# Kernel optimization log

Measured on AMD Instinct MI355X. Metric: run time of the kernel, lower is better.

The kernel has to match this reference:

```python
import jax, jax.numpy as jnp
import numpy as np

N_HEADS = 8
HEAD_D = 64


def setup_inputs() -> dict:
    key = jax.random.key(0)
    ks = jax.random.split(key, 7)
    b, ds, dc = 4, 4096, 256
    ls, lc = 512, 512
    inner = N_HEADS * HEAD_D  # 512
    out_dim = 512
    data = jax.random.normal(ks[0], (b, ds, dc), dtype=jnp.float32)
    latent = jax.random.normal(ks[1], (b, ls, lc), dtype=jnp.float32)
    # torch nn.Linear weights are [out_features, in_features]
    Wq = jax.random.normal(ks[2], (inner, lc), dtype=jnp.float32) * (lc ** -0.5)
    Wk = jax.random.normal(ks[3], (inner, dc), dtype=jnp.float32) * (dc ** -0.5)
    Wv = jax.random.normal(ks[4], (inner, dc), dtype=jnp.float32) * (dc ** -0.5)
    Wo = jax.random.normal(ks[5], (out_dim, inner), dtype=jnp.float32) * (inner ** -0.5)
    bo = jax.random.normal(ks[6], (out_dim,), dtype=jnp.float32) * 0.02
    return {"data": data, "latent": latent, "Wq": Wq, "Wk": Wk, "Wv": Wv, "Wo": Wo, "bo": bo}


def reference(data, latent, Wq, Wk, Wv, Wo, bo):
    b, ds, _ = data.shape
    ls = latent.shape[1]
    scale = HEAD_D ** -0.5
    # projections, split into heads
    Q = (latent @ Wq.T).reshape(b, ls, N_HEADS, HEAD_D)  # [b,ls,h,d]
    K = (data @ Wk.T).reshape(b, ds, N_HEADS, HEAD_D)    # [b,ds,h,d]
    V = (data @ Wv.T).reshape(b, ds, N_HEADS, HEAD_D)
    # logits [b, ds, ls, h]; original broadcasts then sums over head_d -> einsum
    logits = jnp.einsum('blhd,bshd->bslh', Q, K) * scale
    # softmax over key axis (dim 1 = ds), matching attn_logits.softmax(1)
    attn = jax.nn.softmax(logits, axis=1)
    # weighted sum over keys: [b, ls, h, d] -> [b, ls, inner]
    out = jnp.einsum('bshd,bslh->blhd', V, attn).reshape(b, ls, N_HEADS * HEAD_D)
    # output Linear (dropout is identity in eval)
    return out @ Wo.T + bo
```

## Files before the change

kernel.cpp:

```cpp
#include <hip/hip_runtime.h>

typedef __bf16 bf16;
typedef __bf16 bf16x8 __attribute__((ext_vector_type(8)));
typedef float  f32x4  __attribute__((ext_vector_type(4)));


__device__ __forceinline__ bf16x8 cvt8(float4 a, float4 b) {
    bf16x8 r;
    r[0] = (bf16)a.x; r[1] = (bf16)a.y; r[2] = (bf16)a.z; r[3] = (bf16)a.w;
    r[4] = (bf16)b.x; r[5] = (bf16)b.y; r[6] = (bf16)b.z; r[7] = (bf16)b.w;
    return r;
}

__global__ __launch_bounds__(256) void proj_kvq(
    const float* __restrict__ data, const float* __restrict__ latent,
    const float* __restrict__ Wk, const float* __restrict__ Wv, const float* __restrict__ Wq,
    bf16* __restrict__ K_b, bf16* __restrict__ Vt_b, bf16* __restrict__ Q_b)
{
    __shared__ bf16 As[128 * 32];
    __shared__ bf16 Bs[128 * 32];
    const int bx = blockIdx.x;
    const float* A; const float* Bm; bf16* outb;
    int Kdim, mode, m0, n0;
    if (bx < 512)       { A = data;   Bm = Wk; outb = K_b;  Kdim = 256; mode = 0; m0 = (bx & 127) * 128;         n0 = (bx >> 7) * 128; }
    else if (bx < 1024) { int t = bx - 512;  A = data;   Bm = Wv; outb = Vt_b; Kdim = 256; mode = 1; m0 = (t & 127) * 128; n0 = (t >> 7) * 128; }
    else                { int t = bx - 1024; A = latent; Bm = Wq; outb = Q_b;  Kdim = 512; mode = 2; m0 = (t & 15) * 128;  n0 = (t >> 4) * 128; }

    const int tid = threadIdx.x;
    const int wave = tid >> 6, lane = tid & 63;
    const int wm = wave >> 1, wn = wave & 1;
    const int l15 = lane & 15, quad = lane >> 4;
    const int rowA = tid >> 2;
    const int c8 = (tid & 3) * 8;

    const float* Arow0 = A + (size_t)(m0 + rowA) * Kdim + c8;
    const float* Arow1 = A + (size_t)(m0 + 64 + rowA) * Kdim + c8;
    const float* Brow0 = Bm + (size_t)(n0 + rowA) * Kdim + c8;
    const float* Brow1 = Bm + (size_t)(n0 + 64 + rowA) * Kdim + c8;

    f32x4 acc[4][4] = {};
    float4 a00, a01, a10, a11, b00, b01, b10, b11;

#define LOADP(k) do { \
        a00 = *(const float4*)(Arow0 + (k));     a01 = *(const float4*)(Arow0 + (k) + 4); \
        a10 = *(const float4*)(Arow1 + (k));     a11 = *(const float4*)(Arow1 + (k) + 4); \
        b00 = *(const float4*)(Brow0 + (k));     b01 = *(const float4*)(Brow0 + (k) + 4); \
        b10 = *(const float4*)(Brow1 + (k));     b11 = *(const float4*)(Brow1 + (k) + 4); \
    } while (0)

    LOADP(0);

    for (int k0 = 0; k0 < Kdim; k0 += 32) {
        __syncthreads();
        *(bf16x8*)(As + (size_t)tid * 8)        = cvt8(a00, a01);
        *(bf16x8*)(As + 2048 + (size_t)tid * 8) = cvt8(a10, a11);
        *(bf16x8*)(Bs + (size_t)tid * 8)        = cvt8(b00, b01);
        *(bf16x8*)(Bs + 2048 + (size_t)tid * 8) = cvt8(b10, b11);
        if (k0 + 32 < Kdim) LOADP(k0 + 32);
        __syncthreads();

        bf16x8 af[4], bfr[4];
        #pragma unroll
        for (int mt = 0; mt < 4; mt++)
            af[mt] = *(const bf16x8*)(As + (wm * 64 + mt * 16 + l15) * 32 + quad * 8);
        #pragma unroll
        for (int nt = 0; nt < 4; nt++)
            bfr[nt] = *(const bf16x8*)(Bs + (wn * 64 + nt * 16 + l15) * 32 + quad * 8);
        #pragma unroll
        for (int mt = 0; mt < 4; mt++)
            #pragma unroll
            for (int nt = 0; nt < 4; nt++)
                acc[mt][nt] = __builtin_amdgcn_mfma_f32_16x16x32_bf16(af[mt], bfr[nt], acc[mt][nt], 0, 0, 0);
    }
#undef LOADP

    #pragma unroll
    for (int mt = 0; mt < 4; mt++) {
        #pragma unroll
        for (int nt = 0; nt < 4; nt++) {
            #pragma unroll
            for (int r = 0; r < 4; r++) {
                int m = m0 + wm * 64 + mt * 16 + quad * 4 + r;
                int n = n0 + wn * 64 + nt * 16 + l15;
                float v = acc[mt][nt][r];
                if (mode == 0) {
                    outb[(size_t)(((m >> 12) << 3) + (n >> 6)) * 262144 + (m & 4095) * 64 + (n & 63)] = (bf16)v;
                } else if (mode == 1) {
                    outb[(size_t)(((m >> 12) << 3) + (n >> 6)) * 262144 + (n & 63) * 4096 + (m & 4095)] = (bf16)v;
                } else {
                    outb[(size_t)(((m >> 9) << 3) + (n >> 6)) * 32768 + (m & 511) * 64 + (n & 63)] = (bf16)v;
                }
            }
        }
    }
}

#define LDK 72
__global__ __launch_bounds__(256) void flash_attn(
    const bf16* __restrict__ Q, const bf16* __restrict__ K,
    const bf16* __restrict__ Vt, float* __restrict__ Opart, float* __restrict__ lbuf)
{
    __shared__ bf16 Ks[64 * LDK];
    __shared__ bf16 Vs[64 * LDK];
    __shared__ bf16 Ps[4][16 * LDK];

    const int tid = threadIdx.x;
    const int bx = blockIdx.x;
    const int qt = bx >> 7;
    const int bh = (bx & 127) >> 2;
    const int ks = bx & 3;
    const int wave = tid >> 6, lane = tid & 63;
    const int l15 = lane & 15, quad = lane >> 4;

    const bf16* Qb = Q + (size_t)bh * 32768 + (size_t)(qt * 64 + wave * 16 + l15) * 64;
    bf16x8 aq[2];
    aq[0] = *(const bf16x8*)(Qb + quad * 8);
    aq[1] = *(const bf16x8*)(Qb + 32 + quad * 8);

    const bf16* Kb = K + (size_t)bh * 262144;
    const bf16* Vb = Vt + (size_t)bh * 262144;

    f32x4 oacc[4] = {};
    float lpart[4] = {0.f, 0.f, 0.f, 0.f};
    const float scale = 0.125f;

    const int i0 = tid, i1 = tid + 256;
    const int r0 = i0 >> 3, c0 = (i0 & 7) * 8;
    const int r1 = i1 >> 3, c1 = (i1 & 7) * 8;

    const int kstart = ks * 1024, kend = kstart + 1024;

    uint4 pk0 = *(const uint4*)(Kb + (size_t)(kstart + r0) * 64 + c0);
    uint4 pk1 = *(const uint4*)(Kb + (size_t)(kstart + r1) * 64 + c1);
    uint4 pv0 = *(const uint4*)(Vb + (size_t)r0 * 4096 + kstart + c0);
    uint4 pv1 = *(const uint4*)(Vb + (size_t)r1 * 4096 + kstart + c1);

    for (int key0 = kstart; key0 < kend; key0 += 64) {
        __syncthreads();
        *(uint4*)(Ks + r0 * LDK + c0) = pk0;
        *(uint4*)(Ks + r1 * LDK + c1) = pk1;
        *(uint4*)(Vs + r0 * LDK + c0) = pv0;
        *(uint4*)(Vs + r1 * LDK + c1) = pv1;
        if (key0 + 64 < kend) {
            pk0 = *(const uint4*)(Kb + (size_t)(key0 + 64 + r0) * 64 + c0);
            pk1 = *(const uint4*)(Kb + (size_t)(key0 + 64 + r1) * 64 + c1);
            pv0 = *(const uint4*)(Vb + (size_t)r0 * 4096 + key0 + 64 + c0);
            pv1 = *(const uint4*)(Vb + (size_t)r1 * 4096 + key0 + 64 + c1);
        }
        __syncthreads();

        float p[4][4];
        #pragma unroll
        for (int nt = 0; nt < 4; nt++) {
            f32x4 z = {};
            #pragma unroll
            for (int kf = 0; kf < 2; kf++) {
                bf16x8 bk = *(const bf16x8*)(Ks + (nt * 16 + l15) * LDK + kf * 32 + quad * 8);
                z = __builtin_amdgcn_mfma_f32_16x16x32_bf16(aq[kf], bk, z, 0, 0, 0);
            }
            #pragma unroll
            for (int r = 0; r < 4; r++) {
                float e = __expf(z[r] * scale);
                p[r][nt] = e;
                lpart[r] += e;
            }
        }

        #pragma unroll
        for (int r = 0; r < 4; r++)
            #pragma unroll
            for (int nt = 0; nt < 4; nt++)
                Ps[wave][(quad * 4 + r) * LDK + nt * 16 + l15] = (bf16)p[r][nt];

        bf16x8 ap[2];
        ap[0] = *(const bf16x8*)(&Ps[wave][l15 * LDK + quad * 8]);
        ap[1] = *(const bf16x8*)(&Ps[wave][l15 * LDK + 32 + quad * 8]);
        #pragma unroll
        for (int dt = 0; dt < 4; dt++) {
            #pragma unroll
            for (int kf = 0; kf < 2; kf++) {
                bf16x8 bv = *(const bf16x8*)(Vs + (dt * 16 + l15) * LDK + kf * 32 + quad * 8);
                oacc[dt] = __builtin_amdgcn_mfma_f32_16x16x32_bf16(ap[kf], bv, oacc[dt], 0, 0, 0);
            }
        }
    }

    #pragma unroll
    for (int r = 0; r < 4; r++) {
        #pragma unroll
        for (int off = 1; off < 16; off <<= 1) lpart[r] += __shfl_xor(lpart[r], off, 64);
    }

    const int rowbase = bh * 512 + qt * 64 + wave * 16 + quad * 4;
    #pragma unroll
    for (int dt = 0; dt < 4; dt++) {
        #pragma unroll
        for (int r = 0; r < 4; r++) {
            Opart[((size_t)ks * 16384 + rowbase + r) * 64 + dt * 16 + l15] = oacc[dt][r];
        }
    }
    if (l15 == 0) {
        #pragma unroll
        for (int r = 0; r < 4; r++)
            lbuf[(size_t)ks * 16384 + rowbase + r] = lpart[r];
    }
}

__global__ __launch_bounds__(256) void gemm_out(
    const float* __restrict__ Opart, const float* __restrict__ lbuf,
    const float* __restrict__ Wo, const float* __restrict__ bo, float* __restrict__ out)
{
    __shared__ bf16 As[64 * 32];
    __shared__ bf16 Bs[64 * 32];
    const int tid = threadIdx.x;
    const int m0 = blockIdx.x * 64, n0 = blockIdx.y * 64;
    const int wave = tid >> 6, lane = tid & 63;
    const int wm = wave >> 1, wn = wave & 1;
    const int l15 = lane & 15, quad = lane >> 4;
    const int rowA = tid >> 2;
    const int c8 = (tid & 3) * 8;
    const int m = m0 + rowA;
    const int mhi = (m >> 9) << 3, mlo = m & 511;

    f32x4 acc[2][2] = {};
    float4 pa[8]; float pl[4]; float4 pb0, pb1;

    auto loadA = [&](int k0) {
        int kc = k0 + c8;
        int arow = (mhi + (kc >> 6)) * 512 + mlo;
        int d0 = kc & 63;
        #pragma unroll
        for (int ks = 0; ks < 4; ks++) {
            pl[ks] = lbuf[(size_t)ks * 16384 + arow];
            pa[2 * ks]     = *(const float4*)(Opart + ((size_t)ks * 16384 + arow) * 64 + d0);
            pa[2 * ks + 1] = *(const float4*)(Opart + ((size_t)ks * 16384 + arow) * 64 + d0 + 4);
        }
    };
    auto loadB = [&](int k0) {
        pb0 = *(const float4*)(Wo + (size_t)(n0 + rowA) * 512 + k0 + c8);
        pb1 = *(const float4*)(Wo + (size_t)(n0 + rowA) * 512 + k0 + c8 + 4);
    };

    loadA(0); loadB(0);

    for (int k0 = 0; k0 < 512; k0 += 32) {
        __syncthreads();
        {
            float L = pl[0] + pl[1] + pl[2] + pl[3];
            float inv = 1.0f / L;
            float4 s0, s1;
            s0.x = pa[0].x + pa[2].x + pa[4].x + pa[6].x;
            s0.y = pa[0].y + pa[2].y + pa[4].y + pa[6].y;
            s0.z = pa[0].z + pa[2].z + pa[4].z + pa[6].z;
            s0.w = pa[0].w + pa[2].w + pa[4].w + pa[6].w;
            s1.x = pa[1].x + pa[3].x + pa[5].x + pa[7].x;
            s1.y = pa[1].y + pa[3].y + pa[5].y + pa[7].y;
            s1.z = pa[1].z + pa[3].z + pa[5].z + pa[7].z;
            s1.w = pa[1].w + pa[3].w + pa[5].w + pa[7].w;
            s0.x *= inv; s0.y *= inv; s0.z *= inv; s0.w *= inv;
            s1.x *= inv; s1.y *= inv; s1.z *= inv; s1.w *= inv;
            *(bf16x8*)(As + (size_t)tid * 8) = cvt8(s0, s1);
            *(bf16x8*)(Bs + (size_t)tid * 8) = cvt8(pb0, pb1);
        }
        if (k0 + 32 < 512) { loadA(k0 + 32); loadB(k0 + 32); }
        __syncthreads();

        bf16x8 af[2], bfr[2];
        #pragma unroll
        for (int mt = 0; mt < 2; mt++)
            af[mt] = *(const bf16x8*)(As + (wm * 32 + mt * 16 + l15) * 32 + quad * 8);
        #pragma unroll
        for (int nt = 0; nt < 2; nt++)
            bfr[nt] = *(const bf16x8*)(Bs + (wn * 32 + nt * 16 + l15) * 32 + quad * 8);
        #pragma unroll
        for (int mt = 0; mt < 2; mt++)
            #pragma unroll
            for (int nt = 0; nt < 2; nt++)
                acc[mt][nt] = __builtin_amdgcn_mfma_f32_16x16x32_bf16(af[mt], bfr[nt], acc[mt][nt], 0, 0, 0);
    }

    #pragma unroll
    for (int mt = 0; mt < 2; mt++) {
        #pragma unroll
        for (int nt = 0; nt < 2; nt++) {
            #pragma unroll
            for (int r = 0; r < 4; r++) {
                int mm = m0 + wm * 32 + mt * 16 + quad * 4 + r;
                int nn = n0 + wn * 32 + nt * 16 + l15;
                out[(size_t)mm * 512 + nn] = acc[mt][nt][r] + bo[nn];
            }
        }
    }
}

extern "C" void kernel_launch(void* const* d_in, const int* in_sizes, int n_in,
                              void* d_out, int out_size, void* d_ws, size_t ws_size,
                              hipStream_t stream) {
    const float* data   = (const float*)d_in[0];
    const float* latent = (const float*)d_in[1];
    const float* Wq = (const float*)d_in[2];
    const float* Wk = (const float*)d_in[3];
    const float* Wv = (const float*)d_in[4];
    const float* Wo = (const float*)d_in[5];
    const float* bo = (const float*)d_in[6];
    float* out = (float*)d_out;

    bf16* ws = (bf16*)d_ws;
    bf16* Q_b    = ws;
    bf16* K_b    = Q_b + 1048576;
    bf16* Vt_b   = K_b + 8388608;
    float* Opart = (float*)(Vt_b + 8388608);
    float* lbuf  = Opart + 4 * 16384 * 64;

    proj_kvq<<<1088, 256, 0, stream>>>(data, latent, Wk, Wv, Wq, K_b, Vt_b, Q_b);
    flash_attn<<<1024, 256, 0, stream>>>(Q_b, K_b, Vt_b, Opart, lbuf);
    gemm_out<<<dim3(32, 8), 256, 0, stream>>>(Opart, lbuf, Wo, bo, out);
}
```

Measured before the change: 165.6 us.

## Restructure projection GEMM to 512 threads, K-step 64, padded LDS

The K/V/Q projection kernel now runs 8 waves per block instead of 4, each wave computing a 64x32 sub-tile. Each K step grows from 32 to 64 and uses a padded shared-memory row stride of 72 to cut LDS bank conflicts. The register prefetch of the next tile is removed, so global loads are issued at the top of each step without overlapping compute, and each step needs fewer syncs. This trades the software pipelining for more waves per block to hide latency.

Result: slower. 169.2 us (+2.2%).

```diff
diff --git a/kernel.cpp b/kernel.cpp
--- a/kernel.cpp
+++ b/kernel.cpp
@@ -12,13 +12,14 @@
     return r;
 }
 
-__global__ __launch_bounds__(256) void proj_kvq(
+#define LDP 72
+__global__ __launch_bounds__(512) void proj_kvq(
     const float* __restrict__ data, const float* __restrict__ latent,
     const float* __restrict__ Wk, const float* __restrict__ Wv, const float* __restrict__ Wq,
     bf16* __restrict__ K_b, bf16* __restrict__ Vt_b, bf16* __restrict__ Q_b)
 {
-    __shared__ bf16 As[128 * 32];
-    __shared__ bf16 Bs[128 * 32];
+    __shared__ bf16 As[128 * LDP];
+    __shared__ bf16 Bs[128 * LDP];
     const int bx = blockIdx.x;
     const float* A; const float* Bm; bf16* outb;
     int Kdim, mode, m0, n0;
@@ -28,60 +29,60 @@
 
     const int tid = threadIdx.x;
     const int wave = tid >> 6, lane = tid & 63;
-    const int wm = wave >> 1, wn = wave & 1;
+    const int wm = wave >> 2;
+    const int wn = wave & 3;
     const int l15 = lane & 15, quad = lane >> 4;
-    const int rowA = tid >> 2;
-    const int c8 = (tid & 3) * 8;
-
-    const float* Arow0 = A + (size_t)(m0 + rowA) * Kdim + c8;
-    const float* Arow1 = A + (size_t)(m0 + 64 + rowA) * Kdim + c8;
-    const float* Brow0 = Bm + (size_t)(n0 + rowA) * Kdim + c8;
-    const float* Brow1 = Bm + (size_t)(n0 + 64 + rowA) * Kdim + c8;
-
-    f32x4 acc[4][4] = {};
-    float4 a00, a01, a10, a11, b00, b01, b10, b11;
-
-#define LOADP(k) do { \
-        a00 = *(const float4*)(Arow0 + (k));     a01 = *(const float4*)(Arow0 + (k) + 4); \
-        a10 = *(const float4*)(Arow1 + (k));     a11 = *(const float4*)(Arow1 + (k) + 4); \
-        b00 = *(const float4*)(Brow0 + (k));     b01 = *(const float4*)(Brow0 + (k) + 4); \
-        b10 = *(const float4*)(Brow1 + (k));     b11 = *(const float4*)(Brow1 + (k) + 4); \
-    } while (0)
-
-    LOADP(0);
-
-    for (int k0 = 0; k0 < Kdim; k0 += 32) {
-        __syncthreads();
-        *(bf16x8*)(As + (size_t)tid * 8)        = cvt8(a00, a01);
-        *(bf16x8*)(As + 2048 + (size_t)tid * 8) = cvt8(a10, a11);
-        *(bf16x8*)(Bs + (size_t)tid * 8)        = cvt8(b00, b01);
-        *(bf16x8*)(Bs + 2048 + (size_t)tid * 8) = cvt8(b10, b11);
-        if (k0 + 32 < Kdim) LOADP(k0 + 32);
-        __syncthreads();
-
-        bf16x8 af[4], bfr[4];
-        #pragma unroll
-        for (int mt = 0; mt < 4; mt++)
-            af[mt] = *(const bf16x8*)(As + (wm * 64 + mt * 16 + l15) * 32 + quad * 8);
-        #pragma unroll
-        for (int nt = 0; nt < 4; nt++)
-            bfr[nt] = *(const bf16x8*)(Bs + (wn * 64 + nt * 16 + l15) * 32 + quad * 8);
-        #pragma unroll
-        for (int mt = 0; mt < 4; mt++)
-            #pragma unroll
-            for (int nt = 0; nt < 4; nt++)
-                acc[mt][nt] = __builtin_amdgcn_mfma_f32_16x16x32_bf16(af[mt], bfr[nt], acc[mt][nt], 0, 0, 0);
-    }
-#undef LOADP
+    const int rowS = tid >> 2;
+    const int segS = (tid & 3) * 16;
+
+    const float* Arow = A + (size_t)(m0 + rowS) * Kdim + segS;
+    const float* Brow = Bm + (size_t)(n0 + rowS) * Kdim + segS;
+    bf16* AsD = As + rowS * LDP + segS;
+    bf16* BsD = Bs + rowS * LDP + segS;
+
+    f32x4 acc[4][2] = {};
+
+    for (int k0 = 0; k0 < Kdim; k0 += 64) {
+        float4 a0 = *(const float4*)(Arow + k0);
+        float4 a1 = *(const float4*)(Arow + k0 + 4);
+        float4 a2 = *(const float4*)(Arow + k0 + 8);
+        float4 a3 = *(const float4*)(Arow + k0 + 12);
+        float4 b0 = *(const float4*)(Brow + k0);
+        float4 b1 = *(const float4*)(Brow + k0 + 4);
+        float4 b2 = *(const float4*)(Brow + k0 + 8);
+        float4 b3 = *(const float4*)(Brow + k0 + 12);
+        __syncthreads();
+        *(bf16x8*)(AsD)     = cvt8(a0, a1);
+        *(bf16x8*)(AsD + 8) = cvt8(a2, a3);
+        *(bf16x8*)(BsD)     = cvt8(b0, b1);
+        *(bf16x8*)(BsD + 8) = cvt8(b2, b3);
+        __syncthreads();
+
+        #pragma unroll
+        for (int kf = 0; kf < 2; kf++) {
+            bf16x8 af[4], bfr[2];
+            #pragma unroll
+            for (int mt = 0; mt < 4; mt++)
+                af[mt] = *(const bf16x8*)(As + (wm * 64 + mt * 16 + l15) * LDP + kf * 32 + quad * 8);
+            #pragma unroll
+            for (int nt = 0; nt < 2; nt++)
+                bfr[nt] = *(const bf16x8*)(Bs + (wn * 32 + nt * 16 + l15) * LDP + kf * 32 + quad * 8);
+            #pragma unroll
+            for (int mt = 0; mt < 4; mt++)
+                #pragma unroll
+                for (int nt = 0; nt < 2; nt++)
+                    acc[mt][nt] = __builtin_amdgcn_mfma_f32_16x16x32_bf16(af[mt], bfr[nt], acc[mt][nt], 0, 0, 0);
+        }
+    }
 
     #pragma unroll
     for (int mt = 0; mt < 4; mt++) {
         #pragma unroll
-        for (int nt = 0; nt < 4; nt++) {
+        for (int nt = 0; nt < 2; nt++) {
             #pragma unroll
             for (int r = 0; r < 4; r++) {
                 int m = m0 + wm * 64 + mt * 16 + quad * 4 + r;
-                int n = n0 + wn * 64 + nt * 16 + l15;
+                int n = n0 + wn * 32 + nt * 16 + l15;
                 float v = acc[mt][nt][r];
                 if (mode == 0) {
                     outb[(size_t)(((m >> 12) << 3) + (n >> 6)) * 262144 + (m & 4095) * 64 + (n & 63)] = (bf16)v;
@@ -312,7 +313,7 @@
     float* Opart = (float*)(Vt_b + 8388608);
     float* lbuf  = Opart + 4 * 16384 * 64;
 
-    proj_kvq<<<1088, 256, 0, stream>>>(data, latent, Wk, Wv, Wq, K_b, Vt_b, Q_b);
+    proj_kvq<<<1088, 512, 0, stream>>>(data, latent, Wk, Wv, Wq, K_b, Vt_b, Q_b);
     flash_attn<<<1024, 256, 0, stream>>>(Q_b, K_b, Vt_b, Opart, lbuf);
     gemm_out<<<dim3(32, 8), 256, 0, stream>>>(Opart, lbuf, Wo, bo, out);
 }
```

## Pre-cast projection inputs to bf16 and stage GEMM tiles via direct global-to-LDS loads

Applied to the files above, without the earlier changes.

Adds a cast kernel that converts data, latent and the Q/K/V weights to bf16 in workspace before the projection GEMM. The projection kernel then loads bf16 tiles straight into double-buffered LDS using global_load_lds, instead of loading fp32 into registers and converting per tile. This cuts register staging and conversion work in the GEMM and halves the bytes it reads per tile. The cost is an extra kernel launch plus a full read and write pass over the inputs, about 24 MB of traffic. Data is reread by 4 column blocks, so the GEMM-side savings may or may not cover that extra pass.

Result: slower. 171.5 us (+3.6%).

```diff
diff --git a/kernel.cpp b/kernel.cpp
--- a/kernel.cpp
+++ b/kernel.cpp
@@ -5,6 +5,9 @@
 typedef float  f32x4  __attribute__((ext_vector_type(4)));
 
 
+__device__ __forceinline__ unsigned short f2bf(float x) {
+    return __builtin_bit_cast(unsigned short, (bf16)x);
+}
 __device__ __forceinline__ bf16x8 cvt8(float4 a, float4 b) {
     bf16x8 r;
     r[0] = (bf16)a.x; r[1] = (bf16)a.y; r[2] = (bf16)a.z; r[3] = (bf16)a.w;
@@ -12,15 +15,39 @@
     return r;
 }
 
+typedef const __attribute__((address_space(1))) void as1c_void;
+typedef __attribute__((address_space(3))) void as3_void;
+__device__ __forceinline__ void gld16(const bf16* g, bf16* l) {
+    __builtin_amdgcn_global_load_lds((as1c_void*)g, (as3_void*)l, 16, 0, 0);
+}
+
+struct CastArgs {
+    const float* src[5];
+    bf16* dst[5];
+    unsigned cum4[6];
+};
+
+__global__ __launch_bounds__(256) void cast_all(CastArgs a) {
+    unsigned i = blockIdx.x * 256u + threadIdx.x;
+    if (i >= a.cum4[5]) return;
+    int r = 0;
+    while (i >= a.cum4[r + 1]) ++r;
+    unsigned j = i - a.cum4[r];
+    float4 v = ((const float4*)a.src[r])[j];
+    ushort4 o;
+    o.x = f2bf(v.x); o.y = f2bf(v.y); o.z = f2bf(v.z); o.w = f2bf(v.w);
+    *(ushort4*)(a.dst[r] + (size_t)j * 4) = o;
+}
+
 __global__ __launch_bounds__(256) void proj_kvq(
-    const float* __restrict__ data, const float* __restrict__ latent,
-    const float* __restrict__ Wk, const float* __restrict__ Wv, const float* __restrict__ Wq,
+    const bf16* __restrict__ data, const bf16* __restrict__ latent,
+    const bf16* __restrict__ Wk, const bf16* __restrict__ Wv, const bf16* __restrict__ Wq,
     bf16* __restrict__ K_b, bf16* __restrict__ Vt_b, bf16* __restrict__ Q_b)
 {
-    __shared__ bf16 As[128 * 32];
-    __shared__ bf16 Bs[128 * 32];
+    __shared__ bf16 As[2][128 * 32];
+    __shared__ bf16 Bs[2][128 * 32];
     const int bx = blockIdx.x;
-    const float* A; const float* Bm; bf16* outb;
+    const bf16* A; const bf16* Bm; bf16* outb;
     int Kdim, mode, m0, n0;
     if (bx < 512)       { A = data;   Bm = Wk; outb = K_b;  Kdim = 256; mode = 0; m0 = (bx & 127) * 128;         n0 = (bx >> 7) * 128; }
     else if (bx < 1024) { int t = bx - 512;  A = data;   Bm = Wv; outb = Vt_b; Kdim = 256; mode = 1; m0 = (t & 127) * 128; n0 = (t >> 7) * 128; }
@@ -30,49 +57,45 @@
     const int wave = tid >> 6, lane = tid & 63;
     const int wm = wave >> 1, wn = wave & 1;
     const int l15 = lane & 15, quad = lane >> 4;
-    const int rowA = tid >> 2;
-    const int c8 = (tid & 3) * 8;
-
-    const float* Arow0 = A + (size_t)(m0 + rowA) * Kdim + c8;
-    const float* Arow1 = A + (size_t)(m0 + 64 + rowA) * Kdim + c8;
-    const float* Brow0 = Bm + (size_t)(n0 + rowA) * Kdim + c8;
-    const float* Brow1 = Bm + (size_t)(n0 + 64 + rowA) * Kdim + c8;
+
+    const int soff0 = (wave * 32 + (lane >> 2)) * 32 + (lane & 3) * 8;
+    const int soff1 = soff0 + 16 * 32;
+    const bf16* Ag0 = A + (size_t)(m0 + wave * 32 + (lane >> 2)) * Kdim + (lane & 3) * 8;
+    const bf16* Ag1 = Ag0 + 16 * (size_t)Kdim;
+    const bf16* Bg0 = Bm + (size_t)(n0 + wave * 32 + (lane >> 2)) * Kdim + (lane & 3) * 8;
+    const bf16* Bg1 = Bg0 + 16 * (size_t)Kdim;
+
+#define STAGE(k0, c) do { \
+        gld16(Ag0 + (k0), &As[c][soff0]); \
+        gld16(Ag1 + (k0), &As[c][soff1]); \
+        gld16(Bg0 + (k0), &Bs[c][soff0]); \
+        gld16(Bg1 + (k0), &Bs[c][soff1]); \
+    } while (0)
 
     f32x4 acc[4][4] = {};
-    float4 a00, a01, a10, a11, b00, b01, b10, b11;
-
-#define LOADP(k) do { \
-        a00 = *(const float4*)(Arow0 + (k));     a01 = *(const float4*)(Arow0 + (k) + 4); \
-        a10 = *(const float4*)(Arow1 + (k));     a11 = *(const float4*)(Arow1 + (k) + 4); \
-        b00 = *(const float4*)(Brow0 + (k));     b01 = *(const float4*)(Brow0 + (k) + 4); \
-        b10 = *(const float4*)(Brow1 + (k));     b11 = *(const float4*)(Brow1 + (k) + 4); \
-    } while (0)
-
-    LOADP(0);
-
-    for (int k0 = 0; k0 < Kdim; k0 += 32) {
-        __syncthreads();
-        *(bf16x8*)(As + (size_t)tid * 8)        = cvt8(a00, a01);
-        *(bf16x8*)(As + 2048 + (size_t)tid * 8) = cvt8(a10, a11);
-        *(bf16x8*)(Bs + (size_t)tid * 8)        = cvt8(b00, b01);
-        *(bf16x8*)(Bs + 2048 + (size_t)tid * 8) = cvt8(b10, b11);
-        if (k0 + 32 < Kdim) LOADP(k0 + 32);
-        __syncthreads();
+    const int nIter = Kdim >> 5;
+
+    STAGE(0, 0);
+    for (int i = 0; i < nIter; i++) {
+        __syncthreads();
+        if (i + 1 < nIter) STAGE((i + 1) << 5, (i + 1) & 1);
+        const bf16* Ab = &As[i & 1][0];
+        const bf16* Bb = &Bs[i & 1][0];
 
         bf16x8 af[4], bfr[4];
         #pragma unroll
         for (int mt = 0; mt < 4; mt++)
-            af[mt] = *(const bf16x8*)(As + (wm * 64 + mt * 16 + l15) * 32 + quad * 8);
+            af[mt] = *(const bf16x8*)(Ab + (wm * 64 + mt * 16 + l15) * 32 + quad * 8);
         #pragma unroll
         for (int nt = 0; nt < 4; nt++)
-            bfr[nt] = *(const bf16x8*)(Bs + (wn * 64 + nt * 16 + l15) * 32 + quad * 8);
+            bfr[nt] = *(const bf16x8*)(Bb + (wn * 64 + nt * 16 + l15) * 32 + quad * 8);
         #pragma unroll
         for (int mt = 0; mt < 4; mt++)
             #pragma unroll
             for (int nt = 0; nt < 4; nt++)
                 acc[mt][nt] = __builtin_amdgcn_mfma_f32_16x16x32_bf16(af[mt], bfr[nt], acc[mt][nt], 0, 0, 0);
     }
-#undef LOADP
+#undef STAGE
 
     #pragma unroll
     for (int mt = 0; mt < 4; mt++) {
@@ -306,13 +329,32 @@
     float* out = (float*)d_out;
 
     bf16* ws = (bf16*)d_ws;
-    bf16* Q_b    = ws;
-    bf16* K_b    = Q_b + 1048576;
-    bf16* Vt_b   = K_b + 8388608;
-    float* Opart = (float*)(Vt_b + 8388608);
-    float* lbuf  = Opart + 4 * 16384 * 64;
-
-    proj_kvq<<<1088, 256, 0, stream>>>(data, latent, Wk, Wv, Wq, K_b, Vt_b, Q_b);
+    bf16* data_b   = ws;
+    bf16* latent_b = data_b + 4194304;
+    bf16* Wk_b     = latent_b + 1048576;
+    bf16* Wv_b     = Wk_b + 131072;
+    bf16* Wq_b     = Wv_b + 131072;
+    bf16* Q_b      = Wq_b + 262144;
+    bf16* K_b      = Q_b + 1048576;
+    bf16* Vt_b     = K_b + 8388608;
+    float* Opart   = (float*)(Vt_b + 8388608);
+    float* lbuf    = Opart + 4 * 16384 * 64;
+
+    CastArgs ca;
+    const float* srcs[5] = {data, latent, Wk, Wv, Wq};
+    bf16* dsts[5] = {data_b, latent_b, Wk_b, Wv_b, Wq_b};
+    unsigned counts[5] = {4194304u, 1048576u, 131072u, 131072u, 262144u};
+    unsigned cum = 0;
+    for (int i = 0; i < 5; i++) {
+        ca.src[i] = srcs[i];
+        ca.dst[i] = dsts[i];
+        ca.cum4[i] = cum;
+        cum += counts[i] / 4;
+    }
+    ca.cum4[5] = cum;
+    cast_all<<<(cum + 255) / 256, 256, 0, stream>>>(ca);
+
+    proj_kvq<<<1088, 256, 0, stream>>>(data_b, latent_b, Wk_b, Wv_b, Wq_b, K_b, Vt_b, Q_b);
     flash_attn<<<1024, 256, 0, stream>>>(Q_b, K_b, Vt_b, Opart, lbuf);
     gemm_out<<<dim3(32, 8), 256, 0, stream>>>(Opart, lbuf, Wo, bo, out);
 }
```
